# Performance work log

Hardware: AMD Instinct MI355X
Metric: run time of the kernel (lower is better)

## Reference

```python
import jax, jax.numpy as jnp
import numpy as np

B, N, DIN, DOUT = 8, 2048, 512, 512

def setup_inputs() -> dict:
    key = jax.random.key(0)
    kx, ka, kw, kb, kattn = jax.random.split(key, 5)
    x = jax.random.normal(kx, (B, N, DIN), dtype=jnp.float32)
    adjacency_matrix = jax.random.randint(ka, (B, N, N), 0, 2, dtype=jnp.int32)
    # nn.Linear(in,out): weight [out,in], bias [out]
    lim_w = float(np.sqrt(1.0 / DIN))
    W = jax.random.uniform(kw, (DOUT, DIN), minval=-lim_w, maxval=lim_w, dtype=jnp.float32)
    b = jax.random.uniform(kb, (DOUT,), minval=-lim_w, maxval=lim_w, dtype=jnp.float32)
    # xavier_uniform for attn [out,out]
    lim_a = float(np.sqrt(6.0 / (DOUT + DOUT)))
    attn = jax.random.uniform(kattn, (DOUT, DOUT), minval=-lim_a, maxval=lim_a, dtype=jnp.float32)
    return {"x": x, "adjacency_matrix": adjacency_matrix, "W": W, "b": b, "attn": attn}

def reference(x, adjacency_matrix, W, b, attn):
    h = jnp.einsum('bni,oi->bno', x, W) + b                 # [B,N,DOUT]
    ha = jnp.einsum('bmi,ij->bmj', h, attn)                  # h @ attn
    scores = jnp.einsum('bmj,bnj->bmn', ha, h)               # bilinear pairwise scores
    scores = jnp.where(adjacency_matrix == 0, -jnp.inf, scores)
    attn_weights = jax.nn.softmax(scores, axis=-1)           # adjacency-masked softmax
    x_out = jnp.einsum('bmn,bnd->bmd', attn_weights, h)      # weighted aggregation
    return jax.nn.elu(x_out)
```

## Files before the change

### kernel.cpp

```cpp
#include <hip/hip_runtime.h>
#include <cstdint>
#include <cstddef>

typedef unsigned short u16;
using f16x8 = __attribute__((ext_vector_type(8))) _Float16;
using f32x4 = __attribute__((ext_vector_type(4))) float;
using u16x4 = __attribute__((ext_vector_type(4))) unsigned short;

__device__ __forceinline__ u16 f2h(float f) {
  union { _Float16 h; u16 u; } c;
  c.h = (_Float16)f;
  return c.u;
}

__device__ __forceinline__ void gl_lds16(const void* g, void* lds) {
  __builtin_amdgcn_global_load_lds(
      (const __attribute__((address_space(1))) void*)(uintptr_t)g,
      (__attribute__((address_space(3))) void*)(uint32_t)(uintptr_t)lds,
      16, 0, 0);
}

template <int ROWS>
__device__ __forceinline__ void stage_tile(const u16* g, int ldk, u16* lds, int t) {
#pragma unroll
  for (int i = 0; i < ROWS / 64; ++i) {
    const int s = i * 512 + t;
    gl_lds16(g + (size_t)(s >> 3) * ldk + (s & 7) * 8,
             lds + (size_t)(i * 512 + (t & ~63)) * 8);
  }
}

template <int BN, int MODE>
__global__ __launch_bounds__(512) void gemm256(
    const u16* __restrict__ A, const u16* __restrict__ Bt,
    void* __restrict__ Cv, const float* __restrict__ bias,
    int M, int Ncols, int K,
    long long strideA, long long strideB, long long strideC)
{
  constexpr int NF = BN / 64;
  __shared__ __align__(16) u16 sA[2][256 * 64];
  __shared__ __align__(16) u16 sB[2][BN * 64];

  const int bz = blockIdx.z;
  A  += (size_t)bz * strideA;
  Bt += (size_t)bz * strideB;

  const int m0 = blockIdx.y * 256;
  const int n0 = blockIdx.x * BN;
  const int t    = threadIdx.x;
  const int lane = t & 63;
  const int wave = t >> 6;
  const int wm   = (wave >> 2) * 128;
  const int wn   = (wave & 3) * (BN / 4);
  const int lm   = lane & 15;
  const int quad = lane >> 4;

  f32x4 acc[8][NF];
#pragma unroll
  for (int i = 0; i < 8; ++i)
#pragma unroll
    for (int j = 0; j < NF; ++j) acc[i][j] = f32x4{0.f, 0.f, 0.f, 0.f};

  const u16* Ag = A + (size_t)m0 * K;
  const u16* Bg = Bt + (size_t)n0 * K;

  const int nk = K >> 6;
  stage_tile<256>(Ag, K, sA[0], t);
  stage_tile<BN >(Bg, K, sB[0], t);
  __syncthreads();

  for (int kt = 0; kt < nk; ++kt) {
    const int cur = kt & 1;
    if (kt + 1 < nk) {
      stage_tile<256>(Ag + ((kt + 1) << 6), K, sA[cur ^ 1], t);
      stage_tile<BN >(Bg + ((kt + 1) << 6), K, sB[cur ^ 1], t);
    }

    const u16* pA = sA[cur];
    const u16* pB = sB[cur];
    f16x8 bf[NF][2];
#pragma unroll
    for (int nf = 0; nf < NF; ++nf)
#pragma unroll
      for (int ks = 0; ks < 2; ++ks)
        bf[nf][ks] = *(const f16x8*)(pB + (wn + nf * 16 + lm) * 64 + ks * 32 + quad * 8);
#pragma unroll
    for (int mf = 0; mf < 8; ++mf) {
      const u16* ra = pA + (wm + mf * 16 + lm) * 64 + quad * 8;
      f16x8 a0 = *(const f16x8*)(ra);
      f16x8 a1 = *(const f16x8*)(ra + 32);
#pragma unroll
      for (int nf = 0; nf < NF; ++nf) {
        acc[mf][nf] = __builtin_amdgcn_mfma_f32_16x16x32_f16(a0, bf[nf][0], acc[mf][nf], 0, 0, 0);
        acc[mf][nf] = __builtin_amdgcn_mfma_f32_16x16x32_f16(a1, bf[nf][1], acc[mf][nf], 0, 0, 0);
      }
    }
    if (kt + 1 < nk) __syncthreads();
  }

  if (MODE == 0) {
    u16* C = (u16*)Cv + (size_t)bz * strideC;
#pragma unroll
    for (int nf = 0; nf < NF; ++nf) {
      const int col = n0 + wn + nf * 16 + lm;
      const float bv = bias ? bias[col] : 0.f;
#pragma unroll
      for (int mf = 0; mf < 8; ++mf)
#pragma unroll
        for (int r = 0; r < 4; ++r) {
          const int row = m0 + wm + mf * 16 + quad * 4 + r;
          C[(size_t)row * Ncols + col] = f2h(acc[mf][nf][r] + bv);
        }
    }
  } else {
    float* C = (float*)Cv + (size_t)bz * strideC;
#pragma unroll
    for (int nf = 0; nf < NF; ++nf) {
      const int col = n0 + wn + nf * 16 + lm;
#pragma unroll
      for (int mf = 0; mf < 8; ++mf)
#pragma unroll
        for (int r = 0; r < 4; ++r) {
          const int row = m0 + wm + mf * 16 + quad * 4 + r;
          float v = acc[mf][nf][r];
          if (MODE == 2) v = v > 0.f ? v : expm1f(v);
          C[(size_t)row * Ncols + col] = v;
        }
    }
  }
}

__global__ __launch_bounds__(256) void masked_softmax(
    const float* __restrict__ S, const int* __restrict__ adj, u16* __restrict__ P)
{
  const size_t row = blockIdx.x;
  const float* s = S + row * 2048;
  const int*   a = adj + row * 2048;
  u16*         p = P + row * 2048;
  const int t = threadIdx.x;

  float v[8];
#pragma unroll
  for (int i = 0; i < 2; ++i) {
    float4 sv = ((const float4*)s)[t + i * 256];
    int4   av = ((const int4*)a)[t + i * 256];
    v[i * 4 + 0] = av.x ? sv.x : -1e30f;
    v[i * 4 + 1] = av.y ? sv.y : -1e30f;
    v[i * 4 + 2] = av.z ? sv.z : -1e30f;
    v[i * 4 + 3] = av.w ? sv.w : -1e30f;
  }
  float mx = v[0];
#pragma unroll
  for (int i = 1; i < 8; ++i) mx = fmaxf(mx, v[i]);
#pragma unroll
  for (int o = 32; o > 0; o >>= 1) mx = fmaxf(mx, __shfl_xor(mx, o));
  __shared__ float red[4];
  if ((t & 63) == 0) red[t >> 6] = mx;
  __syncthreads();
  mx = fmaxf(fmaxf(red[0], red[1]), fmaxf(red[2], red[3]));
  __syncthreads();

  float e[8]; float sum = 0.f;
#pragma unroll
  for (int i = 0; i < 8; ++i) { e[i] = __expf(v[i] - mx); sum += e[i]; }
#pragma unroll
  for (int o = 32; o > 0; o >>= 1) sum += __shfl_xor(sum, o);
  if ((t & 63) == 0) red[t >> 6] = sum;
  __syncthreads();
  sum = red[0] + red[1] + red[2] + red[3];
  const float inv = 1.f / sum;

#pragma unroll
  for (int i = 0; i < 2; ++i) {
    u16x4 o4;
    o4[0] = f2h(e[i * 4 + 0] * inv);
    o4[1] = f2h(e[i * 4 + 1] * inv);
    o4[2] = f2h(e[i * 4 + 2] * inv);
    o4[3] = f2h(e[i * 4 + 3] * inv);
    ((u16x4*)p)[t + i * 256] = o4;
  }
}

__global__ __launch_bounds__(256) void transpose_u16(
    const u16* __restrict__ in, u16* __restrict__ outp, int R, int C)
{
  __shared__ u16 tile[64][65];
  const size_t base = (size_t)blockIdx.z * R * C;
  const int r0 = blockIdx.y * 64, c0 = blockIdx.x * 64;
  const int t = threadIdx.x;
  const int c = t & 63, rr = t >> 6;
#pragma unroll
  for (int i = 0; i < 16; ++i) {
    const int r = rr + i * 4;
    tile[r][c] = in[base + (size_t)(r0 + r) * C + c0 + c];
  }
  __syncthreads();
  const int rp = t & 63, cc = t >> 6;
#pragma unroll
  for (int i = 0; i < 16; ++i) {
    const int cq = cc + i * 4;
    outp[base + (size_t)(c0 + cq) * R + r0 + rp] = tile[rp][cq];
  }
}

__global__ __launch_bounds__(256) void cvt_f32_f16(
    const float* __restrict__ in, u16* __restrict__ outp, int n4)
{
  const int i = blockIdx.x * 256 + threadIdx.x;
  if (i >= n4) return;
  float4 v = ((const float4*)in)[i];
  u16x4 o; o[0] = f2h(v.x); o[1] = f2h(v.y); o[2] = f2h(v.z); o[3] = f2h(v.w);
  ((u16x4*)outp)[i] = o;
}

__global__ __launch_bounds__(256) void transpose_cvt(
    const float* __restrict__ in, u16* __restrict__ outp, int R, int C)
{
  const int idx = blockIdx.x * 256 + threadIdx.x;
  const int i = idx / C, j = idx % C;
  outp[(size_t)j * R + i] = f2h(in[idx]);
}

extern "C" void kernel_launch(void* const* d_in, const int* in_sizes, int n_in,
                              void* d_out, int out_size, void* d_ws, size_t ws_size,
                              hipStream_t stream) {
  (void)in_sizes; (void)n_in; (void)out_size;
  const float* x    = (const float*)d_in[0];
  const int*   adj  = (const int*)d_in[1];
  const float* W    = (const float*)d_in[2];
  const float* bvec = (const float*)d_in[3];
  const float* attn = (const float*)d_in[4];
  float* out = (float*)d_out;

  constexpr int B = 8, N = 2048, D = 512;
  constexpr size_t MN = (size_t)B * N;

  char* ws = (char*)d_ws;
  size_t off = 0;
  auto take = [&](size_t bytes) -> char* {
    char* p = ws + off;
    off += (bytes + 255) & ~(size_t)255;
    return p;
  };
  u16* xh   = (u16*)take(MN * D * 2);
  u16* Wh   = (u16*)take((size_t)D * D * 2);
  u16* attT = (u16*)take((size_t)D * D * 2);
  u16* h    = (u16*)take(MN * D * 2);
  u16* hT   = (u16*)take(MN * D * 2);
  u16* ha   = (u16*)take(MN * D * 2);

  auto al = [](size_t b) { return (b + 255) & ~(size_t)255; };
  const size_t szSf = al((size_t)B * N * N * 4), szPf = al((size_t)B * N * N * 2);
  const size_t szSb = al((size_t)N * N * 4),     szPb = al((size_t)N * N * 2);
  const bool full  = ws_size >= off + szSf + szPf;
  const bool ok_pb = ws_size >= off + szSb + szPb;
  if (!full && !ok_pb) return;

  cvt_f32_f16<<<dim3((unsigned)(MN * D / 4 / 256)), 256, 0, stream>>>(x, xh, (int)(MN * D / 4));
  cvt_f32_f16<<<dim3(D * D / 4 / 256), 256, 0, stream>>>(W, Wh, D * D / 4);
  transpose_cvt<<<dim3(D * D / 256), 256, 0, stream>>>(attn, attT, D, D);

  gemm256<128, 0><<<dim3(D / 128, MN / 256, 1), 512, 0, stream>>>(
      xh, Wh, h, bvec, (int)MN, D, D, 0, 0, 0);
  transpose_u16<<<dim3(D / 64, N / 64, B), 256, 0, stream>>>(h, hT, N, D);
  gemm256<128, 0><<<dim3(D / 128, MN / 256, 1), 512, 0, stream>>>(
      h, attT, ha, nullptr, (int)MN, D, D, 0, 0, 0);

  if (full) {
    float* S = (float*)take(szSf);
    u16*   P = (u16*)take(szPf);
    gemm256<256, 1><<<dim3(N / 256, N / 256, B), 512, 0, stream>>>(
        ha, h, S, nullptr, N, N, D,
        (long long)N * D, (long long)N * D, (long long)N * N);
    masked_softmax<<<dim3((unsigned)(B * N)), 256, 0, stream>>>(S, adj, P);
    gemm256<128, 2><<<dim3(D / 128, N / 256, B), 512, 0, stream>>>(
        P, hT, out, nullptr, N, D, N,
        (long long)N * N, (long long)D * N, (long long)N * D);
  } else {
    float* S = (float*)take(szSb);
    u16*   P = (u16*)take(szPb);
    for (int b = 0; b < B; ++b) {
      gemm256<256, 1><<<dim3(N / 256, N / 256, 1), 512, 0, stream>>>(
          ha + (size_t)b * N * D, h + (size_t)b * N * D, S, nullptr, N, N, D, 0, 0, 0);
      masked_softmax<<<dim3(N), 256, 0, stream>>>(S, adj + (size_t)b * N * N, P);
      gemm256<128, 2><<<dim3(D / 128, N / 256, 1), 512, 0, stream>>>(
          P, hT + (size_t)b * D * N, out + (size_t)b * N * D, nullptr, N, D, N, 0, 0, 0);
    }
  }
}
```

Before: 432.2 us.

## Rework GEMM mainloop into 4-stage K=32 pipeline with swizzled LDS and raw barriers

Replaces the double-buffered K=64 GEMM loop with a four-buffer K=32 ring that keeps two tiles of global-to-LDS loads in flight. It uses explicit vmcnt waits and bare s_barrier instead of __syncthreads. An XOR swizzle on the LDS column chunk is meant to cut bank conflicts on fragment reads, and launch bounds now request 2 blocks per CU. The aim is to hide global load latency behind MFMA work. The cost is more complex hand-managed synchronization, and the code assumes K is a multiple of 128.

```diff
diff --git a/kernel.cpp b/kernel.cpp
--- a/kernel.cpp
+++ b/kernel.cpp
@@ -20,26 +20,67 @@
       16, 0, 0);
 }
 
+template <int N> __device__ __forceinline__ void vmcnt_wait() {
+  if constexpr (N == 0)      asm volatile("s_waitcnt vmcnt(0)" ::: "memory");
+  else if constexpr (N == 3) asm volatile("s_waitcnt vmcnt(3)" ::: "memory");
+  else if constexpr (N == 4) asm volatile("s_waitcnt vmcnt(4)" ::: "memory");
+  else static_assert(N == 0, "unsupported vmcnt literal");
+}
+
+__device__ __forceinline__ void block_sync() {
+  asm volatile("" ::: "memory");
+  __builtin_amdgcn_s_barrier();
+  asm volatile("" ::: "memory");
+}
+
 template <int ROWS>
-__device__ __forceinline__ void stage_tile(const u16* g, int ldk, u16* lds, int t) {
-#pragma unroll
-  for (int i = 0; i < ROWS / 64; ++i) {
-    const int s = i * 512 + t;
-    gl_lds16(g + (size_t)(s >> 3) * ldk + (s & 7) * 8,
+__device__ __forceinline__ void stage32(const u16* g, int ldk, u16* lds, int t) {
+#pragma unroll
+  for (int i = 0; i < ROWS / 128; ++i) {
+    const int s   = i * 512 + t;
+    const int row = s >> 2;
+    const int gc  = (s & 3) ^ ((s >> 3) & 3);
+    gl_lds16(g + (size_t)row * ldk + gc * 8,
              lds + (size_t)(i * 512 + (t & ~63)) * 8);
   }
 }
 
+template <int NF>
+__device__ __forceinline__ void compute_tile32(
+    const u16* pA, const u16* pB, f32x4 (&acc)[8][NF],
+    int wm, int wn, int lm, int cq)
+{
+  f16x8 bf[NF];
+#pragma unroll
+  for (int nf = 0; nf < NF; ++nf)
+    bf[nf] = *(const f16x8*)(pB + (wn + nf * 16 + lm) * 32 + cq * 8);
+#pragma unroll
+  for (int mf = 0; mf < 8; ++mf) {
+    f16x8 a0 = *(const f16x8*)(pA + (wm + mf * 16 + lm) * 32 + cq * 8);
+#pragma unroll
+    for (int nf = 0; nf < NF; ++nf)
+      acc[mf][nf] = __builtin_amdgcn_mfma_f32_16x16x32_f16(a0, bf[nf], acc[mf][nf], 0, 0, 0);
+  }
+}
+
 template <int BN, int MODE>
-__global__ __launch_bounds__(512) void gemm256(
+__global__ __launch_bounds__(512, 2) void gemm32(
     const u16* __restrict__ A, const u16* __restrict__ Bt,
     void* __restrict__ Cv, const float* __restrict__ bias,
     int M, int Ncols, int K,
     long long strideA, long long strideB, long long strideC)
 {
-  constexpr int NF = BN / 64;
-  __shared__ __align__(16) u16 sA[2][256 * 64];
-  __shared__ __align__(16) u16 sB[2][BN * 64];
+  constexpr int NF  = BN / 64;
+  constexpr int LPT = 2 + BN / 128;
+
+  __shared__ __align__(16) u16 sA0[256 * 32];
+  __shared__ __align__(16) u16 sA1[256 * 32];
+  __shared__ __align__(16) u16 sA2[256 * 32];
+  __shared__ __align__(16) u16 sA3[256 * 32];
+  __shared__ __align__(16) u16 sB0[BN * 32];
+  __shared__ __align__(16) u16 sB1[BN * 32];
+  __shared__ __align__(16) u16 sB2[BN * 32];
+  __shared__ __align__(16) u16 sB3[BN * 32];
 
   const int bz = blockIdx.z;
   A  += (size_t)bz * strideA;
@@ -54,6 +95,7 @@
   const int wn   = (wave & 3) * (BN / 4);
   const int lm   = lane & 15;
   const int quad = lane >> 4;
+  const int cq   = quad ^ ((lm >> 1) & 3);
 
   f32x4 acc[8][NF];
 #pragma unroll
@@ -64,39 +106,48 @@
   const u16* Ag = A + (size_t)m0 * K;
   const u16* Bg = Bt + (size_t)n0 * K;
 
-  const int nk = K >> 6;
-  stage_tile<256>(Ag, K, sA[0], t);
-  stage_tile<BN >(Bg, K, sB[0], t);
-  __syncthreads();
-
-  for (int kt = 0; kt < nk; ++kt) {
-    const int cur = kt & 1;
-    if (kt + 1 < nk) {
-      stage_tile<256>(Ag + ((kt + 1) << 6), K, sA[cur ^ 1], t);
-      stage_tile<BN >(Bg + ((kt + 1) << 6), K, sB[cur ^ 1], t);
-    }
-
-    const u16* pA = sA[cur];
-    const u16* pB = sB[cur];
-    f16x8 bf[NF][2];
-#pragma unroll
-    for (int nf = 0; nf < NF; ++nf)
-#pragma unroll
-      for (int ks = 0; ks < 2; ++ks)
-        bf[nf][ks] = *(const f16x8*)(pB + (wn + nf * 16 + lm) * 64 + ks * 32 + quad * 8);
-#pragma unroll
-    for (int mf = 0; mf < 8; ++mf) {
-      const u16* ra = pA + (wm + mf * 16 + lm) * 64 + quad * 8;
-      f16x8 a0 = *(const f16x8*)(ra);
-      f16x8 a1 = *(const f16x8*)(ra + 32);
-#pragma unroll
-      for (int nf = 0; nf < NF; ++nf) {
-        acc[mf][nf] = __builtin_amdgcn_mfma_f32_16x16x32_f16(a0, bf[nf][0], acc[mf][nf], 0, 0, 0);
-        acc[mf][nf] = __builtin_amdgcn_mfma_f32_16x16x32_f16(a1, bf[nf][1], acc[mf][nf], 0, 0, 0);
-      }
-    }
-    if (kt + 1 < nk) __syncthreads();
-  }
+  const int nk = K >> 5;
+
+  stage32<256>(Ag,      K, sA0, t);  stage32<BN>(Bg,      K, sB0, t);
+  stage32<256>(Ag + 32, K, sA1, t);  stage32<BN>(Bg + 32, K, sB1, t);
+
+  for (int kt = 0; kt < nk - 4; kt += 4) {
+    vmcnt_wait<LPT>(); block_sync();
+    stage32<256>(Ag + (size_t)(kt + 2) * 32, K, sA2, t);
+    stage32<BN >(Bg + (size_t)(kt + 2) * 32, K, sB2, t);
+    compute_tile32<NF>(sA0, sB0, acc, wm, wn, lm, cq);
+
+    vmcnt_wait<LPT>(); block_sync();
+    stage32<256>(Ag + (size_t)(kt + 3) * 32, K, sA3, t);
+    stage32<BN >(Bg + (size_t)(kt + 3) * 32, K, sB3, t);
+    compute_tile32<NF>(sA1, sB1, acc, wm, wn, lm, cq);
+
+    vmcnt_wait<LPT>(); block_sync();
+    stage32<256>(Ag + (size_t)(kt + 4) * 32, K, sA0, t);
+    stage32<BN >(Bg + (size_t)(kt + 4) * 32, K, sB0, t);
+    compute_tile32<NF>(sA2, sB2, acc, wm, wn, lm, cq);
+
+    vmcnt_wait<LPT>(); block_sync();
+    stage32<256>(Ag + (size_t)(kt + 5) * 32, K, sA1, t);
+    stage32<BN >(Bg + (size_t)(kt + 5) * 32, K, sB1, t);
+    compute_tile32<NF>(sA3, sB3, acc, wm, wn, lm, cq);
+  }
+
+  vmcnt_wait<LPT>(); block_sync();
+  stage32<256>(Ag + (size_t)(nk - 2) * 32, K, sA2, t);
+  stage32<BN >(Bg + (size_t)(nk - 2) * 32, K, sB2, t);
+  compute_tile32<NF>(sA0, sB0, acc, wm, wn, lm, cq);
+
+  vmcnt_wait<LPT>(); block_sync();
+  stage32<256>(Ag + (size_t)(nk - 1) * 32, K, sA3, t);
+  stage32<BN >(Bg + (size_t)(nk - 1) * 32, K, sB3, t);
+  compute_tile32<NF>(sA1, sB1, acc, wm, wn, lm, cq);
+
+  vmcnt_wait<LPT>(); block_sync();
+  compute_tile32<NF>(sA2, sB2, acc, wm, wn, lm, cq);
+
+  vmcnt_wait<0>(); block_sync();
+  compute_tile32<NF>(sA3, sB3, acc, wm, wn, lm, cq);
 
   if (MODE == 0) {
     u16* C = (u16*)Cv + (size_t)bz * strideC;
@@ -198,8 +249,8 @@
   const int rp = t & 63, cc = t >> 6;
 #pragma unroll
   for (int i = 0; i < 16; ++i) {
-    const int cq = cc + i * 4;
-    outp[base + (size_t)(c0 + cq) * R + r0 + rp] = tile[rp][cq];
+    const int cq2 = cc + i * 4;
+    outp[base + (size_t)(c0 + cq2) * R + r0 + rp] = tile[rp][cq2];
   }
 }
 
@@ -260,30 +311,30 @@
   cvt_f32_f16<<<dim3(D * D / 4 / 256), 256, 0, stream>>>(W, Wh, D * D / 4);
   transpose_cvt<<<dim3(D * D / 256), 256, 0, stream>>>(attn, attT, D, D);
 
-  gemm256<128, 0><<<dim3(D / 128, MN / 256, 1), 512, 0, stream>>>(
+  gemm32<128, 0><<<dim3(D / 128, MN / 256, 1), 512, 0, stream>>>(
       xh, Wh, h, bvec, (int)MN, D, D, 0, 0, 0);
   transpose_u16<<<dim3(D / 64, N / 64, B), 256, 0, stream>>>(h, hT, N, D);
-  gemm256<128, 0><<<dim3(D / 128, MN / 256, 1), 512, 0, stream>>>(
+  gemm32<128, 0><<<dim3(D / 128, MN / 256, 1), 512, 0, stream>>>(
       h, attT, ha, nullptr, (int)MN, D, D, 0, 0, 0);
 
   if (full) {
     float* S = (float*)take(szSf);
     u16*   P = (u16*)take(szPf);
-    gemm256<256, 1><<<dim3(N / 256, N / 256, B), 512, 0, stream>>>(
+    gemm32<256, 1><<<dim3(N / 256, N / 256, B), 512, 0, stream>>>(
         ha, h, S, nullptr, N, N, D,
         (long long)N * D, (long long)N * D, (long long)N * N);
     masked_softmax<<<dim3((unsigned)(B * N)), 256, 0, stream>>>(S, adj, P);
-    gemm256<128, 2><<<dim3(D / 128, N / 256, B), 512, 0, stream>>>(
+    gemm32<128, 2><<<dim3(D / 128, N / 256, B), 512, 0, stream>>>(
         P, hT, out, nullptr, N, D, N,
         (long long)N * N, (long long)D * N, (long long)N * D);
   } else {
     float* S = (float*)take(szSb);
     u16*   P = (u16*)take(szPb);
     for (int b = 0; b < B; ++b) {
-      gemm256<256, 1><<<dim3(N / 256, N / 256, 1), 512, 0, stream>>>(
+      gemm32<256, 1><<<dim3(N / 256, N / 256, 1), 512, 0, stream>>>(
           ha + (size_t)b * N * D, h + (size_t)b * N * D, S, nullptr, N, N, D, 0, 0, 0);
       masked_softmax<<<dim3(N), 256, 0, stream>>>(S, adj + (size_t)b * N * N, P);
-      gemm256<128, 2><<<dim3(D / 128, N / 256, 1), 512, 0, stream>>>(
+      gemm32<128, 2><<<dim3(D / 128, N / 256, 1), 512, 0, stream>>>(
           P, hT + (size_t)b * D * N, out + (size_t)b * N * D, nullptr, N, D, N, 0, 0, 0);
     }
   }
```

Result: no change. 433.5 us (+0.3%).
